# Optimization experiments

Hardware: AMD Instinct MI355X
Metric: run time of the kernel (lower is better)

## Reference

```python
import jax, jax.numpy as jnp
import numpy as np

B, L, H, E = 4, 2048, 8, 64
S, D = L, E

def setup_inputs() -> dict:
    key = jax.random.key(0)
    kq, kk, kv = jax.random.split(key, 3)
    queries = jax.random.normal(kq, (B, L, H, E), dtype=jnp.float32)
    keys = jax.random.normal(kk, (B, S, H, E), dtype=jnp.float32)
    values = jax.random.normal(kv, (B, S, H, D), dtype=jnp.float32)
    # TriangularCausalMask: True above the diagonal -> masked out
    attn_mask = jnp.broadcast_to(
        jnp.triu(jnp.ones((L, S), dtype=bool), k=1)[None, None], (B, 1, L, S)
    )
    return {"queries": queries, "keys": keys, "values": values, "attn_mask": attn_mask}

def reference(queries, keys, values, attn_mask):
    E_ = queries.shape[-1]
    scale = 1.0 / jnp.sqrt(jnp.float32(E_))
    # scores: [B, H, L, S]
    scores = jnp.einsum('blhe,bshe->bhls', queries, keys)
    scores = jnp.where(attn_mask, -jnp.inf, scores)
    A = jax.nn.softmax(scale * scores, axis=-1)  # dropout p=0.01 omitted (eval/deterministic)
    V = jnp.einsum('bhls,bshd->blhd', A, values)
    return (V, A)
```

## Files before the change

### kernel.cpp

```cpp
#include <hip/hip_runtime.h>
#include <hip/hip_bf16.h>
#include <stdint.h>
#include <stddef.h>

typedef __bf16 bf16;
typedef __attribute__((ext_vector_type(8))) __bf16 bf16x8;
typedef __attribute__((ext_vector_type(4))) float f32x4;
typedef unsigned short u16;
typedef __attribute__((ext_vector_type(4))) u16 u16x4;

#define NB 4
#define NL 2048
#define NH 8
#define NE 64
#define NS 2048
#define ND 64
#define CM 0.18033688011112042f
#define STR 72
#define KBUFB (64 * STR * 2)

__device__ __forceinline__ void barrier_keep_vm() {
    asm volatile("s_waitcnt lgkmcnt(0)" ::: "memory");
    __builtin_amdgcn_s_barrier();
    asm volatile("" ::: "memory");
}

__device__ __forceinline__ void block_map(int bid, int& b, int& h, int& qb) {
    const int x  = bid & 7;
    const int u  = bid >> 3;
    qb = (u < 32) ? (u & 15) : 15 - (u & 15);
    const int bh = x * 4 + (u >> 4);
    b = bh >> 3;
    h = bh & 7;
}

__global__ __launch_bounds__(512, 4)
void attn_fwd(const float* __restrict__ Qg, const float* __restrict__ Kg,
              const float* __restrict__ Vg, float* __restrict__ Og,
              float* __restrict__ Ag)
{
    __shared__ __attribute__((aligned(16))) char smem[6 * KBUFB];

    int b, h, qb; block_map(blockIdx.x, b, h, qb);
    const int q0   = qb * 128;
    const int jmax = 2 * qb + 1;

    const int tid  = threadIdx.x;
    const int wid  = tid >> 6;
    const int lane = tid & 63;
    const int g    = lane >> 4;
    const int li   = lane & 15;
    const int jd   = 2 * qb + (wid >> 2);

    const float* qp = Qg + (((size_t)b * NL + q0 + wid * 16 + li) * NH + h) * NE;
    bf16x8 qf[2];
#pragma unroll
    for (int t = 0; t < 2; ++t) {
        f32x4 x0 = *(const f32x4*)(qp + t * 32 + g * 8);
        f32x4 x1 = *(const f32x4*)(qp + t * 32 + g * 8 + 4);
        bf16x8 v;
#pragma unroll
        for (int e = 0; e < 4; ++e) { v[e] = (bf16)x0[e]; v[4 + e] = (bf16)x1[e]; }
        qf[t] = v;
    }

    float* Abase = Ag + (((size_t)(b * NH + h)) * NL + q0) * NS;

    {
        f32x4 z = {0.f, 0.f, 0.f, 0.f};
        for (int j = jmax + 1; j < 32; ++j) {
            float* tb = Abase + j * 64;
#pragma unroll
            for (int s = 0; s < 4; ++s) {
                int f   = s * 512 + tid;
                int row = f >> 4;
                int c4  = (f & 15) * 4;
                __builtin_nontemporal_store(z, (f32x4*)(tb + (size_t)row * NS + c4));
            }
        }
    }

    const int srow = tid >> 3;
    const int scb  = (tid & 7) * 8;
    const float* kbase = Kg + (((size_t)b * NS + srow) * NH + h) * NE + scb;
    const float* vbase = Vg + (((size_t)b * NS + srow) * NH + h) * ND + scb;

    auto loadK = [&](int j, f32x4 r[2]) {
        const float* src = kbase + (size_t)j * 64 * NH * NE;
        r[0] = *(const f32x4*)(src);
        r[1] = *(const f32x4*)(src + 4);
    };
    auto loadV = [&](int j, f32x4 r[2]) {
        const float* src = vbase + (size_t)j * 64 * NH * ND;
        r[0] = *(const f32x4*)(src);
        r[1] = *(const f32x4*)(src + 4);
    };
    auto writeK = [&](char* buf, const f32x4 r[2]) {
        bf16x8 w;
#pragma unroll
        for (int e = 0; e < 4; ++e) { w[e] = (bf16)r[0][e]; w[4 + e] = (bf16)r[1][e]; }
        *(bf16x8*)((bf16*)buf + srow * STR + scb) = w;
    };
    auto writeV = [&](char* buf, const f32x4 r[2]) {
#pragma unroll
        for (int e = 0; e < 8; ++e) {
            int d    = scb + e;
            int boff = (srow * 2) ^ (d & 48);
            *(bf16*)(buf + (size_t)d * (2 * STR) + boff) = (bf16)r[e >> 2][e & 3];
        }
    };
    auto computeScores = [&](const char* buf, int j, float sv[4][4]) {
        const bf16* kl = (const bf16*)buf;
#pragma unroll
        for (int ct = 0; ct < 4; ++ct) {
            f32x4 a = {0.f, 0.f, 0.f, 0.f};
#pragma unroll
            for (int t = 0; t < 2; ++t) {
                bf16x8 kb = *(const bf16x8*)(kl + (size_t)(ct * 16 + li) * STR + 32 * t + 8 * g);
                a = __builtin_amdgcn_mfma_f32_16x16x32_bf16(qf[t], kb, a, 0, 0, 0);
            }
            if (j == jd) {
#pragma unroll
                for (int r = 0; r < 4; ++r) {
                    int scol = j * 64 + ct * 16 + li;
                    int qrow = q0 + wid * 16 + g * 4 + r;
                    sv[ct][r] = (scol > qrow) ? -1e30f : a[r] * CM;
                }
            } else {
#pragma unroll
                for (int r = 0; r < 4; ++r) sv[ct][r] = a[r] * CM;
            }
        }
    };

    float psum[4] = {0.f, 0.f, 0.f, 0.f};
    {
        f32x4 kr0[2], kr1[2];
        loadK(0, kr0); loadK(1, kr1);
        for (int jj = 0; jj <= qb; ++jj) {
            char* buf0 = smem + ((jj & 1) * 2) * KBUFB;
            writeK(buf0, kr0); writeK(buf0 + KBUFB, kr1);
            if (jj < qb) { loadK(2 * jj + 2, kr0); loadK(2 * jj + 3, kr1); }
            barrier_keep_vm();
#pragma unroll
            for (int t2 = 0; t2 < 2; ++t2) {
                const int j = 2 * jj + t2;
                if (j > jd) continue;
                float sv[4][4];
                computeScores(buf0 + t2 * KBUFB, j, sv);
#pragma unroll
                for (int r = 0; r < 4; ++r) {
                    float s0 = __builtin_amdgcn_exp2f(sv[0][r]) + __builtin_amdgcn_exp2f(sv[1][r]);
                    float s1 = __builtin_amdgcn_exp2f(sv[2][r]) + __builtin_amdgcn_exp2f(sv[3][r]);
                    psum[r] += s0 + s1;
                }
            }
        }
    }

    char* KA = smem;
    char* KB = smem + KBUFB;
    char* VA = smem + 2 * KBUFB;
    char* VB = smem + 3 * KBUFB;
    bf16* pl = (bf16*)(smem + 4 * KBUFB) + wid * 16 * STR;

    f32x4 krA[2], vrA[2], krB[2], vrB[2];
    loadK(0, krA); loadV(0, vrA);
    if (16 <= jmax) { loadK(16, krB); loadV(16, vrB); }

    float vinv[4];
#pragma unroll
    for (int r = 0; r < 4; ++r) {
        float s = psum[r];
#pragma unroll
        for (int mk = 1; mk < 16; mk <<= 1) s += __shfl_xor(s, mk);
        vinv[r] = 1.f / s;
    }

    f32x4 oacc[4];
#pragma unroll
    for (int dt = 0; dt < 4; ++dt) oacc[dt] = (f32x4){0.f, 0.f, 0.f, 0.f};

    barrier_keep_vm();

    const int NT2 = (jmax + 1 < 16) ? jmax + 1 : 16;

    auto doTile = [&](const char* kbuf, const char* vbuf, int j) {
        float* arow = Abase + (size_t)(wid * 16) * NS + j * 64;
        if (j <= jd) {
            float sv[4][4];
            computeScores(kbuf, j, sv);
#pragma unroll
            for (int ct = 0; ct < 4; ++ct)
#pragma unroll
                for (int r = 0; r < 4; ++r) {
                    float p = __builtin_amdgcn_exp2f(sv[ct][r]) * vinv[r];
                    pl[(size_t)(g * 4 + r) * STR + ct * 16 + li] = (bf16)p;
                }
            asm volatile("s_waitcnt lgkmcnt(0)" ::: "memory");
            __builtin_amdgcn_sched_barrier(0);

#pragma unroll
            for (int s = 0; s < 4; ++s) {
                int row = g + s * 4;
                u16x4 pw = *(const u16x4*)(pl + (size_t)row * STR + li * 4);
                f32x4 o;
#pragma unroll
                for (int e = 0; e < 4; ++e) {
                    uint32_t w = ((uint32_t)pw[e]) << 16;
                    o[e] = __builtin_bit_cast(float, w);
                }
                *(f32x4*)(arow + (size_t)row * NS + li * 4) = o;
            }
#pragma unroll
            for (int t = 0; t < 2; ++t) {
                bf16x8 pa = *(const bf16x8*)(pl + (size_t)li * STR + 32 * t + 8 * g);
#pragma unroll
                for (int dt = 0; dt < 4; ++dt) {
                    bf16x8 vb = *(const bf16x8*)(vbuf
                                  + (size_t)(dt * 16 + li) * (2 * STR)
                                  + ((64 * t + 16 * g) ^ (dt * 16 & 48)));
                    oacc[dt] = __builtin_amdgcn_mfma_f32_16x16x32_bf16(pa, vb, oacc[dt], 0, 0, 0);
                }
            }
        } else {
            f32x4 z = {0.f, 0.f, 0.f, 0.f};
#pragma unroll
            for (int s = 0; s < 4; ++s) {
                int row = g + s * 4;
                *(f32x4*)(arow + (size_t)row * NS + li * 4) = z;
            }
        }
    };

    for (int t = 0; t < NT2; ++t) {
        const bool stagedB = (16 + t <= jmax);
        writeK(KA, krA); writeV(VA, vrA);
        if (stagedB) { writeK(KB, krB); writeV(VB, vrB); }
        barrier_keep_vm();

        doTile(KA, VA, t);
        if (t + 1 < NT2) { loadK(t + 1, krA); loadV(t + 1, vrA); }
        if (stagedB) {
            doTile(KB, VB, 16 + t);
            if (16 + t + 1 <= jmax) { loadK(17 + t, krB); loadV(17 + t, vrB); }
        }
        barrier_keep_vm();
    }

    float* scr = (float*)smem + wid * 1024;
#pragma unroll
    for (int dt = 0; dt < 4; ++dt)
#pragma unroll
        for (int r = 0; r < 4; ++r)
            scr[(g * 4 + r) * 64 + dt * 16 + li] = oacc[dt][r];
    asm volatile("s_waitcnt lgkmcnt(0)" ::: "memory");
    __builtin_amdgcn_sched_barrier(0);
#pragma unroll
    for (int s = 0; s < 4; ++s) {
        int row = g + s * 4;
        f32x4 o = *(const f32x4*)(scr + row * 64 + li * 4);
        float* op = Og + (((size_t)b * NL + q0 + wid * 16 + row) * NH + h) * ND + li * 4;
        __builtin_nontemporal_store(o, (f32x4*)op);
    }
}

extern "C" void kernel_launch(void* const* d_in, const int* in_sizes, int n_in,
                              void* d_out, int out_size, void* d_ws, size_t ws_size,
                              hipStream_t stream) {
    (void)in_sizes; (void)n_in; (void)out_size; (void)d_ws; (void)ws_size;
    const float* Q = (const float*)d_in[0];
    const float* K = (const float*)d_in[1];
    const float* V = (const float*)d_in[2];
    float* out = (float*)d_out;
    float* Og  = out;
    float* Ag  = out + (size_t)NB * NL * NH * ND;

    attn_fwd<<<dim3(512), dim3(512), 0, stream>>>(Q, K, V, Og, Ag);
}
```

Measured before the change: 161.5 us.

## Replace dual-stream tile loop with single double-buffered loop and nontemporal A stores

Replaces the paired A/B tile schedule, which processed tiles t and 16+t per iteration with two barriers, by a single loop over all tiles. Consecutive tiles alternate between two LDS buffers, so each iteration needs only one barrier and the next K/V tile is loaded while the current one is computed. The zero-fill of the fully masked attention region is moved after the first K/V load so those loads are in flight during the fill. Stores of the attention matrix become nontemporal. The change halves the in-flight register prefetch, which may expose more global-load latency per tile.

```diff
diff --git a/kernel.cpp b/kernel.cpp
--- a/kernel.cpp
+++ b/kernel.cpp
@@ -25,15 +25,6 @@
     asm volatile("" ::: "memory");
 }
 
-__device__ __forceinline__ void block_map(int bid, int& b, int& h, int& qb) {
-    const int x  = bid & 7;
-    const int u  = bid >> 3;
-    qb = (u < 32) ? (u & 15) : 15 - (u & 15);
-    const int bh = x * 4 + (u >> 4);
-    b = bh >> 3;
-    h = bh & 7;
-}
-
 __global__ __launch_bounds__(512, 4)
 void attn_fwd(const float* __restrict__ Qg, const float* __restrict__ Kg,
               const float* __restrict__ Vg, float* __restrict__ Og,
@@ -41,7 +32,13 @@
 {
     __shared__ __attribute__((aligned(16))) char smem[6 * KBUFB];
 
-    int b, h, qb; block_map(blockIdx.x, b, h, qb);
+    const int bid = blockIdx.x;
+    const int x   = bid & 7;
+    const int u   = bid >> 3;
+    const int qb  = (u < 32) ? (u & 15) : 15 - (u & 15);
+    const int bh  = x * 4 + (u >> 4);
+    const int b   = bh >> 3;
+    const int h   = bh & 7;
     const int q0   = qb * 128;
     const int jmax = 2 * qb + 1;
 
@@ -64,21 +61,7 @@
         qf[t] = v;
     }
 
-    float* Abase = Ag + (((size_t)(b * NH + h)) * NL + q0) * NS;
-
-    {
-        f32x4 z = {0.f, 0.f, 0.f, 0.f};
-        for (int j = jmax + 1; j < 32; ++j) {
-            float* tb = Abase + j * 64;
-#pragma unroll
-            for (int s = 0; s < 4; ++s) {
-                int f   = s * 512 + tid;
-                int row = f >> 4;
-                int c4  = (f & 15) * 4;
-                __builtin_nontemporal_store(z, (f32x4*)(tb + (size_t)row * NS + c4));
-            }
-        }
-    }
+    float* Abase = Ag + (((size_t)bh) * NL + q0) * NS;
 
     const int srow = tid >> 3;
     const int scb  = (tid & 7) * 8;
@@ -158,15 +141,23 @@
         }
     }
 
-    char* KA = smem;
-    char* KB = smem + KBUFB;
-    char* VA = smem + 2 * KBUFB;
-    char* VB = smem + 3 * KBUFB;
-    bf16* pl = (bf16*)(smem + 4 * KBUFB) + wid * 16 * STR;
-
-    f32x4 krA[2], vrA[2], krB[2], vrB[2];
-    loadK(0, krA); loadV(0, vrA);
-    if (16 <= jmax) { loadK(16, krB); loadV(16, vrB); }
+    f32x4 kr[2], vr[2];
+    loadK(0, kr);
+    loadV(0, vr);
+
+    {
+        f32x4 z = {0.f, 0.f, 0.f, 0.f};
+        for (int j = jmax + 1; j < 32; ++j) {
+            float* tb = Abase + j * 64;
+#pragma unroll
+            for (int s = 0; s < 4; ++s) {
+                int f   = s * 512 + tid;
+                int row = f >> 4;
+                int c4  = (f & 15) * 4;
+                __builtin_nontemporal_store(z, (f32x4*)(tb + (size_t)row * NS + c4));
+            }
+        }
+    }
 
     float vinv[4];
 #pragma unroll
@@ -181,15 +172,23 @@
 #pragma unroll
     for (int dt = 0; dt < 4; ++dt) oacc[dt] = (f32x4){0.f, 0.f, 0.f, 0.f};
 
+    bf16* pl = (bf16*)(smem + 4 * KBUFB) + wid * 16 * STR;
+
     barrier_keep_vm();
 
-    const int NT2 = (jmax + 1 < 16) ? jmax + 1 : 16;
-
-    auto doTile = [&](const char* kbuf, const char* vbuf, int j) {
+    for (int j = 0; j <= jmax; ++j) {
+        char* kb   = smem + (j & 1) * KBUFB;
+        char* vbuf = smem + (2 + (j & 1)) * KBUFB;
+        writeK(kb, kr);
+        writeV(vbuf, vr);
+        if (j < jmax) { loadK(j + 1, kr); loadV(j + 1, vr); }
+        barrier_keep_vm();
+
         float* arow = Abase + (size_t)(wid * 16) * NS + j * 64;
+
         if (j <= jd) {
             float sv[4][4];
-            computeScores(kbuf, j, sv);
+            computeScores(kb, j, sv);
 #pragma unroll
             for (int ct = 0; ct < 4; ++ct)
 #pragma unroll
@@ -210,8 +209,9 @@
                     uint32_t w = ((uint32_t)pw[e]) << 16;
                     o[e] = __builtin_bit_cast(float, w);
                 }
-                *(f32x4*)(arow + (size_t)row * NS + li * 4) = o;
-            }
+                __builtin_nontemporal_store(o, (f32x4*)(arow + (size_t)row * NS + li * 4));
+            }
+
 #pragma unroll
             for (int t = 0; t < 2; ++t) {
                 bf16x8 pa = *(const bf16x8*)(pl + (size_t)li * STR + 32 * t + 8 * g);
@@ -228,26 +228,12 @@
 #pragma unroll
             for (int s = 0; s < 4; ++s) {
                 int row = g + s * 4;
-                *(f32x4*)(arow + (size_t)row * NS + li * 4) = z;
-            }
-        }
-    };
-
-    for (int t = 0; t < NT2; ++t) {
-        const bool stagedB = (16 + t <= jmax);
-        writeK(KA, krA); writeV(VA, vrA);
-        if (stagedB) { writeK(KB, krB); writeV(VB, vrB); }
-        barrier_keep_vm();
-
-        doTile(KA, VA, t);
-        if (t + 1 < NT2) { loadK(t + 1, krA); loadV(t + 1, vrA); }
-        if (stagedB) {
-            doTile(KB, VB, 16 + t);
-            if (16 + t + 1 <= jmax) { loadK(17 + t, krB); loadV(17 + t, vrB); }
-        }
-        barrier_keep_vm();
-    }
-
+                __builtin_nontemporal_store(z, (f32x4*)(arow + (size_t)row * NS + li * 4));
+            }
+        }
+    }
+
+    barrier_keep_vm();
     float* scr = (float*)smem + wid * 1024;
 #pragma unroll
     for (int dt = 0; dt < 4; ++dt)
```

Result: faster. 134.1 us, median of 2 (-17.0%).
